# Optimization experiments

Measured on AMD Instinct MI355X. Metric: run time of the kernel, lower is better.

Reference implementation:

```python
import jax, jax.numpy as jnp
import numpy as np

GAMMA = 2.0

def setup_inputs() -> dict:
    key = jax.random.key(0)
    k1, k2, k3, k4 = jax.random.split(key, 4)
    B, N, D, C = 4, 512, 128, 10
    x = jax.random.normal(k1, (B, N, D), dtype=jnp.float32)
    span = jax.random.randint(k2, (B, N, N), 0, C, dtype=jnp.int32)
    seqlen = jax.random.randint(k3, (B,), 1, N + 1, dtype=jnp.int32)
    W = jax.random.truncated_normal(k4, -2.0, 2.0, (D, C), dtype=jnp.float32) * 0.02
    b = jnp.zeros((C,), dtype=jnp.float32)
    return {"x": x, "span": span, "seqlen": seqlen, "W": W, "b": b}

def reference(x, span, seqlen, W, b):
    B, N, D = x.shape
    # pairwise tile-multiply: xx[b,i,j,d] = x[b,i,d] * x[b,j,d]
    xx = x[:, :, None, :] * x[:, None, :, :]            # [B,N,N,D]
    logits = jnp.einsum('bijd,dc->bijc', xx, W) + b     # [B,N,N,C]
    sm = jax.nn.softmax(logits, axis=-1)
    # focal loss: gather prob of true class
    prob = jnp.take_along_axis(sm, span[..., None].astype(jnp.int32), axis=-1)[..., 0]
    loss_map = -jnp.power(1.0 - prob, GAMMA) * jnp.log(prob)  # [B,N,N]
    predict = jnp.argmax(sm, axis=-1).astype(jnp.int32)
    # sequence mask [B,N] -> pairwise [B,N,N]
    row = jnp.arange(N)[None, :] < seqlen[:, None]       # [B,N] bool
    val = row[:, None, :] & row[:, :, None]              # [B,N,N]
    valf = val.astype(jnp.float32)
    seqlen2sum = jnp.sum(jnp.square(seqlen.astype(jnp.float32)))
    loss = jnp.sum(loss_map * valf) / seqlen2sum
    predict = predict * val.astype(jnp.int32)
    accuracy = jnp.sum((predict == span).astype(jnp.float32) * valf) / seqlen2sum
    tp = jnp.sum(((predict == span) & (span > 0)).astype(jnp.float32))
    tn = jnp.sum(((predict != span) & (span > 0)).astype(jnp.float32))
    fp = jnp.sum(((predict > 0) & (span <= 0) & val).astype(jnp.float32))
    return (predict, tp, tn, fp, loss, accuracy)
```

## Files before the change

### kernel.cpp

```cpp
#include <hip/hip_runtime.h>
#include <math.h>

#define NB 4
#define NN 512
#define ND 128
#define NC 10
#define NT 32
#define MREP 2
#define NBLK_M (NB*NT*4)

typedef short    bf16x8 __attribute__((ext_vector_type(8)));
typedef unsigned u32x4  __attribute__((ext_vector_type(4)));
typedef float    f32x4  __attribute__((ext_vector_type(4)));

static __device__ __forceinline__ unsigned pack_trunc(float a, float b) {
    unsigned ua = __builtin_bit_cast(unsigned, a);
    unsigned ub = __builtin_bit_cast(unsigned, b);
    return (ua >> 16) | (ub & 0xFFFF0000u);
}

__global__ __launch_bounds__(256) void w2ner_fused(
    const float* __restrict__ x, const int* __restrict__ span,
    const int* __restrict__ seqlen, const float* __restrict__ Wm,
    const float* __restrict__ bias, float* __restrict__ out,
    float* __restrict__ accum)
{
    __shared__ u32x4 sB[40 * 64];
    __shared__ float sRed[4 * 5];

    const int tid = threadIdx.x;
    const int blk = blockIdx.x;
    const int q  = blk & 3;
    const int Tj = (blk >> 2) & 31;
    const int b  = blk >> 7;
    const int wv = tid >> 6, l = tid & 63;
    const int jl = l & 15, kg = l >> 4;
    const int Ti0 = q * 8 + wv * MREP;
    const int j  = Tj * 16 + jl;
    const int sl = seqlen[b];
    const float* xb = x + (size_t)b * NN * ND;

    int sp[MREP][4];
    #pragma unroll
    for (int m = 0; m < MREP; ++m) {
        const int ib = (Ti0 + m) * 16 + kg * 4;
        #pragma unroll
        for (int r = 0; r < 4; ++r)
            sp[m][r] = span[(size_t)b * NN * NN + (size_t)(ib + r) * NN + j];
    }

    {
        const int d0w = 32 * wv + 8 * kg;
        float xjv[8];
        *(float4*)&xjv[0] = *(const float4*)(xb + (size_t)j * ND + d0w);
        *(float4*)&xjv[4] = *(const float4*)(xb + (size_t)j * ND + d0w + 4);
        u32x4 yw[NC];
        #pragma unroll
        for (int e2 = 0; e2 < 4; ++e2) {
            float wb[20];
            const float4* wp = (const float4*)(Wm + (size_t)(d0w + 2 * e2) * NC);
            #pragma unroll
            for (int t5 = 0; t5 < 5; ++t5) *(float4*)&wb[4 * t5] = wp[t5];
            const float x0 = xjv[2 * e2], x1 = xjv[2 * e2 + 1];
            #pragma unroll
            for (int c = 0; c < NC; ++c)
                yw[c][e2] = pack_trunc(x0 * wb[c], x1 * wb[10 + c]);
        }
        #pragma unroll
        for (int c = 0; c < NC; ++c)
            sB[(wv * NC + c) * 64 + l] = yw[c];
    }
    __syncthreads();

    f32x4 acc[MREP][NC];
    #pragma unroll
    for (int m = 0; m < MREP; ++m)
        #pragma unroll
        for (int c = 0; c < NC; ++c) acc[m][c] = (f32x4){0.f, 0.f, 0.f, 0.f};

    #pragma unroll
    for (int g = 0; g < 4; ++g) {
        const int d0 = 32 * g + 8 * kg;
        bf16x8 ah[MREP], al[MREP];
        #pragma unroll
        for (int m = 0; m < MREP; ++m) {
            const int irow = (Ti0 + m) * 16 + jl;
            float xiv[8];
            *(float4*)&xiv[0] = *(const float4*)(xb + (size_t)irow * ND + d0);
            *(float4*)&xiv[4] = *(const float4*)(xb + (size_t)irow * ND + d0 + 4);
            u32x4 ahw, alw;
            #pragma unroll
            for (int e2 = 0; e2 < 4; ++e2) {
                const float a0 = xiv[2 * e2], a1 = xiv[2 * e2 + 1];
                const unsigned u0 = __builtin_bit_cast(unsigned, a0) & 0xFFFF0000u;
                const unsigned u1 = __builtin_bit_cast(unsigned, a1) & 0xFFFF0000u;
                const float h0 = __builtin_bit_cast(float, u0);
                const float h1 = __builtin_bit_cast(float, u1);
                ahw[e2] = (u0 >> 16) | u1;
                alw[e2] = pack_trunc(a0 - h0, a1 - h1);
            }
            ah[m] = __builtin_bit_cast(bf16x8, ahw);
            al[m] = __builtin_bit_cast(bf16x8, alw);
        }
        #pragma unroll
        for (int c = 0; c < NC; ++c) {
            const bf16x8 bh = __builtin_bit_cast(bf16x8, sB[(g * NC + c) * 64 + l]);
            #pragma unroll
            for (int m = 0; m < MREP; ++m) {
                acc[m][c] = __builtin_amdgcn_mfma_f32_16x16x32_bf16(ah[m], bh, acc[m][c], 0, 0, 0);
                acc[m][c] = __builtin_amdgcn_mfma_f32_16x16x32_bf16(al[m], bh, acc[m][c], 0, 0, 0);
            }
        }
    }

    float lsum = 0.f, accn = 0.f, tpn = 0.f, tnn = 0.f, fpn = 0.f;
    #pragma unroll
    for (int m = 0; m < MREP; ++m) {
        const int ib = (Ti0 + m) * 16 + kg * 4;
        #pragma unroll
        for (int r = 0; r < 4; ++r) {
            const int i = ib + r;
            float L[NC];
            #pragma unroll
            for (int c = 0; c < NC; ++c) L[c] = acc[m][c][r] + bias[c];
            int am = 0; float mx = L[0];
            #pragma unroll
            for (int c = 1; c < NC; ++c) { if (L[c] > mx) { mx = L[c]; am = c; } }
            float e[NC]; float s = 0.f;
            #pragma unroll
            for (int c = 0; c < NC; ++c) { e[c] = __expf(L[c] - mx); s += e[c]; }
            const int spv = sp[m][r];
            float lsp = L[0], esp = e[0];
            #pragma unroll
            for (int c = 1; c < NC; ++c) {
                lsp = (spv == c) ? L[c] : lsp;
                esp = (spv == c) ? e[c] : esp;
            }
            const float inv  = __builtin_amdgcn_rcpf(s);
            const float lp   = (lsp - mx) - __logf(s);
            const float prob = esp * inv;
            const float om   = 1.f - prob;
            const float lm   = -(om * om) * lp;
            const bool v = (i < sl) && (j < sl);
            const int pred = v ? am : 0;
            out[(size_t)b * NN * NN + (size_t)i * NN + j] = (float)pred;
            if (v) { lsum += lm; if (pred == spv) accn += 1.f; }
            if (spv > 0) { if (pred == spv) tpn += 1.f; else tnn += 1.f; }
            else if (pred > 0 && v) fpn += 1.f;
        }
    }

    float vals[5] = { lsum, accn, tpn, tnn, fpn };
    #pragma unroll
    for (int k = 0; k < 5; ++k) {
        float vv = vals[k];
        for (int o = 32; o > 0; o >>= 1) vv += __shfl_down(vv, o);
        vals[k] = vv;
    }
    if (l == 0) {
        #pragma unroll
        for (int k = 0; k < 5; ++k) sRed[wv * 5 + k] = vals[k];
    }
    __syncthreads();
    if (tid < 5) {
        float t = sRed[tid] + sRed[5 + tid] + sRed[10 + tid] + sRed[15 + tid];
        accum[(size_t)blk * 5 + tid] = t;
    }
}

__global__ __launch_bounds__(256) void w2ner_final(
    const int* __restrict__ seqlen, const float* __restrict__ accum,
    float* __restrict__ out)
{
    __shared__ float sP[4][5];
    const int tid = threadIdx.x;
    float part[5] = {0.f, 0.f, 0.f, 0.f, 0.f};
    for (int r = tid; r < NBLK_M; r += 256) {
        #pragma unroll
        for (int k = 0; k < 5; ++k) part[k] += accum[(size_t)r * 5 + k];
    }
    #pragma unroll
    for (int k = 0; k < 5; ++k) {
        float v = part[k];
        for (int o = 32; o > 0; o >>= 1) v += __shfl_down(v, o);
        part[k] = v;
    }
    const int wave = tid >> 6;
    const int lane = tid & 63;
    if (lane == 0) {
        #pragma unroll
        for (int k = 0; k < 5; ++k) sP[wave][k] = part[k];
    }
    __syncthreads();
    if (tid == 0) {
        float t[5];
        #pragma unroll
        for (int k = 0; k < 5; ++k) t[k] = sP[0][k] + sP[1][k] + sP[2][k] + sP[3][k];
        float s2 = 0.f;
        for (int k = 0; k < NB; ++k) { float s = (float)seqlen[k]; s2 += s * s; }
        const size_t base = (size_t)NB * NN * NN;
        out[base + 0] = t[2];
        out[base + 1] = t[3];
        out[base + 2] = t[4];
        out[base + 3] = t[0] / s2;
        out[base + 4] = t[1] / s2;
    }
}

extern "C" void kernel_launch(void* const* d_in, const int* in_sizes, int n_in,
                              void* d_out, int out_size, void* d_ws, size_t ws_size,
                              hipStream_t stream) {
    const float* x      = (const float*)d_in[0];
    const int*   span   = (const int*)d_in[1];
    const int*   seqlen = (const int*)d_in[2];
    const float* Wm     = (const float*)d_in[3];
    const float* bias   = (const float*)d_in[4];
    float* out   = (float*)d_out;
    float* accum = (float*)d_ws;

    w2ner_fused<<<dim3(NBLK_M), 256, 0, stream>>>(x, span, seqlen, Wm, bias, out, accum);
    w2ner_final<<<1, 256, 0, stream>>>(seqlen, accum, out);
}
```

Baseline: 23.90 us.

## Fuse final reduction via last-block counter and compute B operand in registers

```diff
diff --git a/kernel.cpp b/kernel.cpp
--- a/kernel.cpp
+++ b/kernel.cpp
@@ -23,11 +23,10 @@
     const float* __restrict__ x, const int* __restrict__ span,
     const int* __restrict__ seqlen, const float* __restrict__ Wm,
     const float* __restrict__ bias, float* __restrict__ out,
-    float* __restrict__ accum)
+    float* __restrict__ accum, unsigned* __restrict__ counter)
 {
-    __shared__ u32x4 sB[40 * 64];
     __shared__ float sRed[4 * 5];
-
+    __shared__ unsigned sLast;
     const int tid = threadIdx.x;
     const int blk = blockIdx.x;
     const int q  = blk & 3;
@@ -39,6 +38,7 @@
     const int j  = Tj * 16 + jl;
     const int sl = seqlen[b];
     const float* xb = x + (size_t)b * NN * ND;
+    const size_t sb = (size_t)b * NN * NN;
 
     int sp[MREP][4];
     #pragma unroll
@@ -46,41 +46,21 @@
         const int ib = (Ti0 + m) * 16 + kg * 4;
         #pragma unroll
         for (int r = 0; r < 4; ++r)
-            sp[m][r] = span[(size_t)b * NN * NN + (size_t)(ib + r) * NN + j];
-    }
-
-    {
-        const int d0w = 32 * wv + 8 * kg;
-        float xjv[8];
-        *(float4*)&xjv[0] = *(const float4*)(xb + (size_t)j * ND + d0w);
-        *(float4*)&xjv[4] = *(const float4*)(xb + (size_t)j * ND + d0w + 4);
-        u32x4 yw[NC];
-        #pragma unroll
-        for (int e2 = 0; e2 < 4; ++e2) {
-            float wb[20];
-            const float4* wp = (const float4*)(Wm + (size_t)(d0w + 2 * e2) * NC);
-            #pragma unroll
-            for (int t5 = 0; t5 < 5; ++t5) *(float4*)&wb[4 * t5] = wp[t5];
-            const float x0 = xjv[2 * e2], x1 = xjv[2 * e2 + 1];
-            #pragma unroll
-            for (int c = 0; c < NC; ++c)
-                yw[c][e2] = pack_trunc(x0 * wb[c], x1 * wb[10 + c]);
-        }
-        #pragma unroll
-        for (int c = 0; c < NC; ++c)
-            sB[(wv * NC + c) * 64 + l] = yw[c];
-    }
-    __syncthreads();
+            sp[m][r] = span[sb + (size_t)(ib + r) * NN + j];
+    }
 
     f32x4 acc[MREP][NC];
     #pragma unroll
-    for (int m = 0; m < MREP; ++m)
-        #pragma unroll
-        for (int c = 0; c < NC; ++c) acc[m][c] = (f32x4){0.f, 0.f, 0.f, 0.f};
+    for (int c = 0; c < NC; ++c) {
+        const float bc = bias[c];
+        #pragma unroll
+        for (int m = 0; m < MREP; ++m) acc[m][c] = (f32x4){bc, bc, bc, bc};
+    }
 
     #pragma unroll
     for (int g = 0; g < 4; ++g) {
         const int d0 = 32 * g + 8 * kg;
+
         bf16x8 ah[MREP], al[MREP];
         #pragma unroll
         for (int m = 0; m < MREP; ++m) {
@@ -94,17 +74,33 @@
                 const float a0 = xiv[2 * e2], a1 = xiv[2 * e2 + 1];
                 const unsigned u0 = __builtin_bit_cast(unsigned, a0) & 0xFFFF0000u;
                 const unsigned u1 = __builtin_bit_cast(unsigned, a1) & 0xFFFF0000u;
-                const float h0 = __builtin_bit_cast(float, u0);
-                const float h1 = __builtin_bit_cast(float, u1);
                 ahw[e2] = (u0 >> 16) | u1;
-                alw[e2] = pack_trunc(a0 - h0, a1 - h1);
+                alw[e2] = pack_trunc(a0 - __builtin_bit_cast(float, u0),
+                                     a1 - __builtin_bit_cast(float, u1));
             }
             ah[m] = __builtin_bit_cast(bf16x8, ahw);
             al[m] = __builtin_bit_cast(bf16x8, alw);
         }
+
+        float xjv[8];
+        *(float4*)&xjv[0] = *(const float4*)(xb + (size_t)j * ND + d0);
+        *(float4*)&xjv[4] = *(const float4*)(xb + (size_t)j * ND + d0 + 4);
+        u32x4 yw[NC];
+        #pragma unroll
+        for (int e2 = 0; e2 < 4; ++e2) {
+            float wb[20];
+            const float4* wp = (const float4*)(Wm + (size_t)(d0 + 2 * e2) * NC);
+            #pragma unroll
+            for (int t5 = 0; t5 < 5; ++t5) *(float4*)&wb[4 * t5] = wp[t5];
+            const float x0 = xjv[2 * e2], x1 = xjv[2 * e2 + 1];
+            #pragma unroll
+            for (int c = 0; c < NC; ++c)
+                yw[c][e2] = pack_trunc(x0 * wb[c], x1 * wb[10 + c]);
+        }
+
         #pragma unroll
         for (int c = 0; c < NC; ++c) {
-            const bf16x8 bh = __builtin_bit_cast(bf16x8, sB[(g * NC + c) * 64 + l]);
+            const bf16x8 bh = __builtin_bit_cast(bf16x8, yw[c]);
             #pragma unroll
             for (int m = 0; m < MREP; ++m) {
                 acc[m][c] = __builtin_amdgcn_mfma_f32_16x16x32_bf16(ah[m], bh, acc[m][c], 0, 0, 0);
@@ -122,7 +118,7 @@
             const int i = ib + r;
             float L[NC];
             #pragma unroll
-            for (int c = 0; c < NC; ++c) L[c] = acc[m][c][r] + bias[c];
+            for (int c = 0; c < NC; ++c) L[c] = acc[m][c][r];
             int am = 0; float mx = L[0];
             #pragma unroll
             for (int c = 1; c < NC; ++c) { if (L[c] > mx) { mx = L[c]; am = c; } }
@@ -143,7 +139,7 @@
             const float lm   = -(om * om) * lp;
             const bool v = (i < sl) && (j < sl);
             const int pred = v ? am : 0;
-            out[(size_t)b * NN * NN + (size_t)i * NN + j] = (float)pred;
+            out[sb + (size_t)i * NN + j] = (float)pred;
             if (v) { lsum += lm; if (pred == spv) accn += 1.f; }
             if (spv > 0) { if (pred == spv) tpn += 1.f; else tnn += 1.f; }
             else if (pred > 0 && v) fpn += 1.f;
@@ -163,47 +159,46 @@
     }
     __syncthreads();
     if (tid < 5) {
-        float t = sRed[tid] + sRed[5 + tid] + sRed[10 + tid] + sRed[15 + tid];
-        accum[(size_t)blk * 5 + tid] = t;
-    }
-}
-
-__global__ __launch_bounds__(256) void w2ner_final(
-    const int* __restrict__ seqlen, const float* __restrict__ accum,
-    float* __restrict__ out)
-{
-    __shared__ float sP[4][5];
-    const int tid = threadIdx.x;
-    float part[5] = {0.f, 0.f, 0.f, 0.f, 0.f};
-    for (int r = tid; r < NBLK_M; r += 256) {
-        #pragma unroll
-        for (int k = 0; k < 5; ++k) part[k] += accum[(size_t)r * 5 + k];
-    }
-    #pragma unroll
-    for (int k = 0; k < 5; ++k) {
-        float v = part[k];
-        for (int o = 32; o > 0; o >>= 1) v += __shfl_down(v, o);
-        part[k] = v;
-    }
-    const int wave = tid >> 6;
-    const int lane = tid & 63;
-    if (lane == 0) {
-        #pragma unroll
-        for (int k = 0; k < 5; ++k) sP[wave][k] = part[k];
-    }
+        accum[(size_t)blk * 5 + tid] =
+            sRed[tid] + sRed[5 + tid] + sRed[10 + tid] + sRed[15 + tid];
+    }
+
+    __threadfence();
+    if (tid == 0) sLast = (atomicAdd(counter, 1u) == NBLK_M - 1u) ? 1u : 0u;
     __syncthreads();
-    if (tid == 0) {
-        float t[5];
-        #pragma unroll
-        for (int k = 0; k < 5; ++k) t[k] = sP[0][k] + sP[1][k] + sP[2][k] + sP[3][k];
-        float s2 = 0.f;
-        for (int k = 0; k < NB; ++k) { float s = (float)seqlen[k]; s2 += s * s; }
-        const size_t base = (size_t)NB * NN * NN;
-        out[base + 0] = t[2];
-        out[base + 1] = t[3];
-        out[base + 2] = t[4];
-        out[base + 3] = t[0] / s2;
-        out[base + 4] = t[1] / s2;
+    if (sLast) {
+        __threadfence();
+        float part[5] = {0.f, 0.f, 0.f, 0.f, 0.f};
+        for (int r2 = tid; r2 < NBLK_M; r2 += 256) {
+            #pragma unroll
+            for (int k = 0; k < 5; ++k) part[k] += accum[(size_t)r2 * 5 + k];
+        }
+        #pragma unroll
+        for (int k = 0; k < 5; ++k) {
+            float vv = part[k];
+            for (int o = 32; o > 0; o >>= 1) vv += __shfl_down(vv, o);
+            part[k] = vv;
+        }
+        __syncthreads();
+        if (l == 0) {
+            #pragma unroll
+            for (int k = 0; k < 5; ++k) sRed[wv * 5 + k] = part[k];
+        }
+        __syncthreads();
+        if (tid == 0) {
+            float t[5];
+            #pragma unroll
+            for (int k = 0; k < 5; ++k)
+                t[k] = sRed[k] + sRed[5 + k] + sRed[10 + k] + sRed[15 + k];
+            float s2 = 0.f;
+            for (int k = 0; k < NB; ++k) { float s = (float)seqlen[k]; s2 += s * s; }
+            const size_t base = (size_t)NB * NN * NN;
+            out[base + 0] = t[2];
+            out[base + 1] = t[3];
+            out[base + 2] = t[4];
+            out[base + 3] = t[0] / s2;
+            out[base + 4] = t[1] / s2;
+        }
     }
 }
 
@@ -216,8 +211,12 @@
     const float* Wm     = (const float*)d_in[3];
     const float* bias   = (const float*)d_in[4];
     float* out   = (float*)d_out;
-    float* accum = (float*)d_ws;
-
-    w2ner_fused<<<dim3(NBLK_M), 256, 0, stream>>>(x, span, seqlen, Wm, bias, out, accum);
-    w2ner_final<<<1, 256, 0, stream>>>(seqlen, accum, out);
+
+    char* ws = (char*)d_ws;
+    float*    accum   = (float*)ws;
+    unsigned* counter = (unsigned*)(ws + NBLK_M * 5 * sizeof(float));
+
+    hipMemsetAsync(counter, 0, sizeof(unsigned), stream);
+    w2ner_fused<<<dim3(NBLK_M), 256, 0, stream>>>(x, span, seqlen, Wm, bias,
+                                                  out, accum, counter);
 }
```

Result: slower. 66.60 us (+178.7%).

## Split D-reduction across wave pairs and double block count

Applied to the files above, without the earlier changes.

```diff
diff --git a/kernel.cpp b/kernel.cpp
--- a/kernel.cpp
+++ b/kernel.cpp
@@ -6,8 +6,7 @@
 #define ND 128
 #define NC 10
 #define NT 32
-#define MREP 2
-#define NBLK_M (NB*NT*4)
+#define NBLK_M (NB*NT*8)
 
 typedef short    bf16x8 __attribute__((ext_vector_type(8)));
 typedef unsigned u32x4  __attribute__((ext_vector_type(4)));
@@ -25,65 +24,47 @@
     const float* __restrict__ bias, float* __restrict__ out,
     float* __restrict__ accum)
 {
-    __shared__ u32x4 sB[40 * 64];
+    __shared__ f32x4 sEx[NC][2][64];
     __shared__ float sRed[4 * 5];
 
     const int tid = threadIdx.x;
     const int blk = blockIdx.x;
-    const int q  = blk & 3;
-    const int Tj = (blk >> 2) & 31;
-    const int b  = blk >> 7;
+    const int b   = blk >> 8;
+    const int rem = blk & 255;
+    const int Tj  = rem >> 3;
+    const int ig  = rem & 7;
     const int wv = tid >> 6, l = tid & 63;
+    const int pair = wv >> 1, h = wv & 1;
     const int jl = l & 15, kg = l >> 4;
-    const int Ti0 = q * 8 + wv * MREP;
+    const int Ti0 = ig * 4 + pair * 2;
+    const int Tf  = Ti0 + h;
     const int j  = Tj * 16 + jl;
     const int sl = seqlen[b];
     const float* xb = x + (size_t)b * NN * ND;
-
-    int sp[MREP][4];
-    #pragma unroll
-    for (int m = 0; m < MREP; ++m) {
-        const int ib = (Ti0 + m) * 16 + kg * 4;
-        #pragma unroll
-        for (int r = 0; r < 4; ++r)
-            sp[m][r] = span[(size_t)b * NN * NN + (size_t)(ib + r) * NN + j];
-    }
-
-    {
-        const int d0w = 32 * wv + 8 * kg;
-        float xjv[8];
-        *(float4*)&xjv[0] = *(const float4*)(xb + (size_t)j * ND + d0w);
-        *(float4*)&xjv[4] = *(const float4*)(xb + (size_t)j * ND + d0w + 4);
-        u32x4 yw[NC];
-        #pragma unroll
-        for (int e2 = 0; e2 < 4; ++e2) {
-            float wb[20];
-            const float4* wp = (const float4*)(Wm + (size_t)(d0w + 2 * e2) * NC);
-            #pragma unroll
-            for (int t5 = 0; t5 < 5; ++t5) *(float4*)&wb[4 * t5] = wp[t5];
-            const float x0 = xjv[2 * e2], x1 = xjv[2 * e2 + 1];
-            #pragma unroll
-            for (int c = 0; c < NC; ++c)
-                yw[c][e2] = pack_trunc(x0 * wb[c], x1 * wb[10 + c]);
-        }
-        #pragma unroll
-        for (int c = 0; c < NC; ++c)
-            sB[(wv * NC + c) * 64 + l] = yw[c];
-    }
-    __syncthreads();
-
-    f32x4 acc[MREP][NC];
-    #pragma unroll
-    for (int m = 0; m < MREP; ++m)
-        #pragma unroll
-        for (int c = 0; c < NC; ++c) acc[m][c] = (f32x4){0.f, 0.f, 0.f, 0.f};
-
-    #pragma unroll
-    for (int g = 0; g < 4; ++g) {
+    const size_t sb = (size_t)b * NN * NN;
+
+    const int ibf = Tf * 16 + kg * 4;
+    int sp[4];
+    #pragma unroll
+    for (int r = 0; r < 4; ++r)
+        sp[r] = span[sb + (size_t)(ibf + r) * NN + j];
+
+    f32x4 acc[2][NC];
+    #pragma unroll
+    for (int c = 0; c < NC; ++c) {
+        const float bc = (h == 0) ? bias[c] : 0.f;
+        acc[0][c] = (f32x4){bc, bc, bc, bc};
+        acc[1][c] = (f32x4){bc, bc, bc, bc};
+    }
+
+    #pragma unroll
+    for (int gi = 0; gi < 2; ++gi) {
+        const int g  = 2 * h + gi;
         const int d0 = 32 * g + 8 * kg;
-        bf16x8 ah[MREP], al[MREP];
-        #pragma unroll
-        for (int m = 0; m < MREP; ++m) {
+
+        bf16x8 ah[2], al[2];
+        #pragma unroll
+        for (int m = 0; m < 2; ++m) {
             const int irow = (Ti0 + m) * 16 + jl;
             float xiv[8];
             *(float4*)&xiv[0] = *(const float4*)(xb + (size_t)irow * ND + d0);
@@ -94,60 +75,94 @@
                 const float a0 = xiv[2 * e2], a1 = xiv[2 * e2 + 1];
                 const unsigned u0 = __builtin_bit_cast(unsigned, a0) & 0xFFFF0000u;
                 const unsigned u1 = __builtin_bit_cast(unsigned, a1) & 0xFFFF0000u;
-                const float h0 = __builtin_bit_cast(float, u0);
-                const float h1 = __builtin_bit_cast(float, u1);
                 ahw[e2] = (u0 >> 16) | u1;
-                alw[e2] = pack_trunc(a0 - h0, a1 - h1);
+                alw[e2] = pack_trunc(a0 - __builtin_bit_cast(float, u0),
+                                     a1 - __builtin_bit_cast(float, u1));
             }
             ah[m] = __builtin_bit_cast(bf16x8, ahw);
             al[m] = __builtin_bit_cast(bf16x8, alw);
         }
+
+        float xjv[8];
+        *(float4*)&xjv[0] = *(const float4*)(xb + (size_t)j * ND + d0);
+        *(float4*)&xjv[4] = *(const float4*)(xb + (size_t)j * ND + d0 + 4);
+        u32x4 yw[NC];
+        #pragma unroll
+        for (int e2 = 0; e2 < 4; ++e2) {
+            float wb[20];
+            const float4* wp = (const float4*)(Wm + (size_t)(d0 + 2 * e2) * NC);
+            #pragma unroll
+            for (int t5 = 0; t5 < 5; ++t5) *(float4*)&wb[4 * t5] = wp[t5];
+            const float x0 = xjv[2 * e2], x1 = xjv[2 * e2 + 1];
+            #pragma unroll
+            for (int c = 0; c < NC; ++c)
+                yw[c][e2] = pack_trunc(x0 * wb[c], x1 * wb[10 + c]);
+        }
+
         #pragma unroll
         for (int c = 0; c < NC; ++c) {
-            const bf16x8 bh = __builtin_bit_cast(bf16x8, sB[(g * NC + c) * 64 + l]);
-            #pragma unroll
-            for (int m = 0; m < MREP; ++m) {
+            const bf16x8 bh = __builtin_bit_cast(bf16x8, yw[c]);
+            #pragma unroll
+            for (int m = 0; m < 2; ++m) {
                 acc[m][c] = __builtin_amdgcn_mfma_f32_16x16x32_bf16(ah[m], bh, acc[m][c], 0, 0, 0);
                 acc[m][c] = __builtin_amdgcn_mfma_f32_16x16x32_bf16(al[m], bh, acc[m][c], 0, 0, 0);
             }
         }
     }
 
+    if (h == 0) {
+        #pragma unroll
+        for (int c = 0; c < NC; ++c) sEx[c][pair][l] = acc[1][c];
+    }
+    __syncthreads();
+    if (h == 1) {
+        #pragma unroll
+        for (int c = 0; c < NC; ++c) {
+            const f32x4 t = sEx[c][pair][l];
+            acc[1][c] += t;
+            sEx[c][pair][l] = acc[0][c];
+        }
+    }
+    __syncthreads();
+    if (h == 0) {
+        #pragma unroll
+        for (int c = 0; c < NC; ++c) acc[0][c] += sEx[c][pair][l];
+    } else {
+        #pragma unroll
+        for (int c = 0; c < NC; ++c) acc[0][c] = acc[1][c];
+    }
+
     float lsum = 0.f, accn = 0.f, tpn = 0.f, tnn = 0.f, fpn = 0.f;
     #pragma unroll
-    for (int m = 0; m < MREP; ++m) {
-        const int ib = (Ti0 + m) * 16 + kg * 4;
-        #pragma unroll
-        for (int r = 0; r < 4; ++r) {
-            const int i = ib + r;
-            float L[NC];
-            #pragma unroll
-            for (int c = 0; c < NC; ++c) L[c] = acc[m][c][r] + bias[c];
-            int am = 0; float mx = L[0];
-            #pragma unroll
-            for (int c = 1; c < NC; ++c) { if (L[c] > mx) { mx = L[c]; am = c; } }
-            float e[NC]; float s = 0.f;
-            #pragma unroll
-            for (int c = 0; c < NC; ++c) { e[c] = __expf(L[c] - mx); s += e[c]; }
-            const int spv = sp[m][r];
-            float lsp = L[0], esp = e[0];
-            #pragma unroll
-            for (int c = 1; c < NC; ++c) {
-                lsp = (spv == c) ? L[c] : lsp;
-                esp = (spv == c) ? e[c] : esp;
-            }
-            const float inv  = __builtin_amdgcn_rcpf(s);
-            const float lp   = (lsp - mx) - __logf(s);
-            const float prob = esp * inv;
-            const float om   = 1.f - prob;
-            const float lm   = -(om * om) * lp;
-            const bool v = (i < sl) && (j < sl);
-            const int pred = v ? am : 0;
-            out[(size_t)b * NN * NN + (size_t)i * NN + j] = (float)pred;
-            if (v) { lsum += lm; if (pred == spv) accn += 1.f; }
-            if (spv > 0) { if (pred == spv) tpn += 1.f; else tnn += 1.f; }
-            else if (pred > 0 && v) fpn += 1.f;
-        }
+    for (int r = 0; r < 4; ++r) {
+        const int i = ibf + r;
+        float L[NC];
+        #pragma unroll
+        for (int c = 0; c < NC; ++c) L[c] = acc[0][c][r];
+        int am = 0; float mx = L[0];
+        #pragma unroll
+        for (int c = 1; c < NC; ++c) { if (L[c] > mx) { mx = L[c]; am = c; } }
+        float e[NC]; float s = 0.f;
+        #pragma unroll
+        for (int c = 0; c < NC; ++c) { e[c] = __expf(L[c] - mx); s += e[c]; }
+        const int spv = sp[r];
+        float lsp = L[0], esp = e[0];
+        #pragma unroll
+        for (int c = 1; c < NC; ++c) {
+            lsp = (spv == c) ? L[c] : lsp;
+            esp = (spv == c) ? e[c] : esp;
+        }
+        const float inv  = __builtin_amdgcn_rcpf(s);
+        const float lp   = (lsp - mx) - __logf(s);
+        const float prob = esp * inv;
+        const float om   = 1.f - prob;
+        const float lm   = -(om * om) * lp;
+        const bool v = (i < sl) && (j < sl);
+        const int pred = v ? am : 0;
+        out[sb + (size_t)i * NN + j] = (float)pred;
+        if (v) { lsum += lm; if (pred == spv) accn += 1.f; }
+        if (spv > 0) { if (pred == spv) tpn += 1.f; else tnn += 1.f; }
+        else if (pred > 0 && v) fpn += 1.f;
     }
 
     float vals[5] = { lsum, accn, tpn, tnn, fpn };
@@ -163,8 +178,8 @@
     }
     __syncthreads();
     if (tid < 5) {
-        float t = sRed[tid] + sRed[5 + tid] + sRed[10 + tid] + sRed[15 + tid];
-        accum[(size_t)blk * 5 + tid] = t;
+        accum[(size_t)blk * 5 + tid] =
+            sRed[tid] + sRed[5 + tid] + sRed[10 + tid] + sRed[15 + tid];
     }
 }
 
```

Result: slower. 27.83 us (+16.5%).

## Drop split-bf16 low term, compute B operand in registers, transpose partials

Applied to the files above, without the earlier changes.

```diff
diff --git a/kernel.cpp b/kernel.cpp
--- a/kernel.cpp
+++ b/kernel.cpp
@@ -13,10 +13,10 @@
 typedef unsigned u32x4  __attribute__((ext_vector_type(4)));
 typedef float    f32x4  __attribute__((ext_vector_type(4)));
 
-static __device__ __forceinline__ unsigned pack_trunc(float a, float b) {
-    unsigned ua = __builtin_bit_cast(unsigned, a);
-    unsigned ub = __builtin_bit_cast(unsigned, b);
-    return (ua >> 16) | (ub & 0xFFFF0000u);
+static __device__ __forceinline__ unsigned pack_bf2(float a, float b) {
+    unsigned short la = __builtin_bit_cast(unsigned short, (__bf16)a);
+    unsigned short hb = __builtin_bit_cast(unsigned short, (__bf16)b);
+    return (unsigned)la | ((unsigned)hb << 16);
 }
 
 __global__ __launch_bounds__(256) void w2ner_fused(
@@ -25,9 +25,7 @@
     const float* __restrict__ bias, float* __restrict__ out,
     float* __restrict__ accum)
 {
-    __shared__ u32x4 sB[40 * 64];
     __shared__ float sRed[4 * 5];
-
     const int tid = threadIdx.x;
     const int blk = blockIdx.x;
     const int q  = blk & 3;
@@ -39,6 +37,7 @@
     const int j  = Tj * 16 + jl;
     const int sl = seqlen[b];
     const float* xb = x + (size_t)b * NN * ND;
+    const size_t sb = (size_t)b * NN * NN;
 
     int sp[MREP][4];
     #pragma unroll
@@ -46,70 +45,57 @@
         const int ib = (Ti0 + m) * 16 + kg * 4;
         #pragma unroll
         for (int r = 0; r < 4; ++r)
-            sp[m][r] = span[(size_t)b * NN * NN + (size_t)(ib + r) * NN + j];
-    }
-
-    {
-        const int d0w = 32 * wv + 8 * kg;
-        float xjv[8];
-        *(float4*)&xjv[0] = *(const float4*)(xb + (size_t)j * ND + d0w);
-        *(float4*)&xjv[4] = *(const float4*)(xb + (size_t)j * ND + d0w + 4);
-        u32x4 yw[NC];
-        #pragma unroll
-        for (int e2 = 0; e2 < 4; ++e2) {
-            float wb[20];
-            const float4* wp = (const float4*)(Wm + (size_t)(d0w + 2 * e2) * NC);
-            #pragma unroll
-            for (int t5 = 0; t5 < 5; ++t5) *(float4*)&wb[4 * t5] = wp[t5];
-            const float x0 = xjv[2 * e2], x1 = xjv[2 * e2 + 1];
-            #pragma unroll
-            for (int c = 0; c < NC; ++c)
-                yw[c][e2] = pack_trunc(x0 * wb[c], x1 * wb[10 + c]);
-        }
-        #pragma unroll
-        for (int c = 0; c < NC; ++c)
-            sB[(wv * NC + c) * 64 + l] = yw[c];
-    }
-    __syncthreads();
+            sp[m][r] = span[sb + (size_t)(ib + r) * NN + j];
+    }
 
     f32x4 acc[MREP][NC];
     #pragma unroll
-    for (int m = 0; m < MREP; ++m)
-        #pragma unroll
-        for (int c = 0; c < NC; ++c) acc[m][c] = (f32x4){0.f, 0.f, 0.f, 0.f};
+    for (int c = 0; c < NC; ++c) {
+        const float bc = bias[c];
+        #pragma unroll
+        for (int m = 0; m < MREP; ++m) acc[m][c] = (f32x4){bc, bc, bc, bc};
+    }
 
     #pragma unroll
     for (int g = 0; g < 4; ++g) {
         const int d0 = 32 * g + 8 * kg;
-        bf16x8 ah[MREP], al[MREP];
+
+        bf16x8 ah[MREP];
         #pragma unroll
         for (int m = 0; m < MREP; ++m) {
             const int irow = (Ti0 + m) * 16 + jl;
             float xiv[8];
             *(float4*)&xiv[0] = *(const float4*)(xb + (size_t)irow * ND + d0);
             *(float4*)&xiv[4] = *(const float4*)(xb + (size_t)irow * ND + d0 + 4);
-            u32x4 ahw, alw;
-            #pragma unroll
-            for (int e2 = 0; e2 < 4; ++e2) {
-                const float a0 = xiv[2 * e2], a1 = xiv[2 * e2 + 1];
-                const unsigned u0 = __builtin_bit_cast(unsigned, a0) & 0xFFFF0000u;
-                const unsigned u1 = __builtin_bit_cast(unsigned, a1) & 0xFFFF0000u;
-                const float h0 = __builtin_bit_cast(float, u0);
-                const float h1 = __builtin_bit_cast(float, u1);
-                ahw[e2] = (u0 >> 16) | u1;
-                alw[e2] = pack_trunc(a0 - h0, a1 - h1);
-            }
+            u32x4 ahw;
+            #pragma unroll
+            for (int e2 = 0; e2 < 4; ++e2)
+                ahw[e2] = pack_bf2(xiv[2 * e2], xiv[2 * e2 + 1]);
             ah[m] = __builtin_bit_cast(bf16x8, ahw);
-            al[m] = __builtin_bit_cast(bf16x8, alw);
-        }
+        }
+
+        float xjv[8];
+        *(float4*)&xjv[0] = *(const float4*)(xb + (size_t)j * ND + d0);
+        *(float4*)&xjv[4] = *(const float4*)(xb + (size_t)j * ND + d0 + 4);
+        u32x4 yw[NC];
+        #pragma unroll
+        for (int e2 = 0; e2 < 4; ++e2) {
+            float wb[20];
+            const float4* wp = (const float4*)(Wm + (size_t)(d0 + 2 * e2) * NC);
+            #pragma unroll
+            for (int t5 = 0; t5 < 5; ++t5) *(float4*)&wb[4 * t5] = wp[t5];
+            const float x0 = xjv[2 * e2], x1 = xjv[2 * e2 + 1];
+            #pragma unroll
+            for (int c = 0; c < NC; ++c)
+                yw[c][e2] = pack_bf2(x0 * wb[c], x1 * wb[10 + c]);
+        }
+
         #pragma unroll
         for (int c = 0; c < NC; ++c) {
-            const bf16x8 bh = __builtin_bit_cast(bf16x8, sB[(g * NC + c) * 64 + l]);
-            #pragma unroll
-            for (int m = 0; m < MREP; ++m) {
+            const bf16x8 bh = __builtin_bit_cast(bf16x8, yw[c]);
+            #pragma unroll
+            for (int m = 0; m < MREP; ++m)
                 acc[m][c] = __builtin_amdgcn_mfma_f32_16x16x32_bf16(ah[m], bh, acc[m][c], 0, 0, 0);
-                acc[m][c] = __builtin_amdgcn_mfma_f32_16x16x32_bf16(al[m], bh, acc[m][c], 0, 0, 0);
-            }
         }
     }
 
@@ -122,7 +108,7 @@
             const int i = ib + r;
             float L[NC];
             #pragma unroll
-            for (int c = 0; c < NC; ++c) L[c] = acc[m][c][r] + bias[c];
+            for (int c = 0; c < NC; ++c) L[c] = acc[m][c][r];
             int am = 0; float mx = L[0];
             #pragma unroll
             for (int c = 1; c < NC; ++c) { if (L[c] > mx) { mx = L[c]; am = c; } }
@@ -143,7 +129,7 @@
             const float lm   = -(om * om) * lp;
             const bool v = (i < sl) && (j < sl);
             const int pred = v ? am : 0;
-            out[(size_t)b * NN * NN + (size_t)i * NN + j] = (float)pred;
+            out[sb + (size_t)i * NN + j] = (float)pred;
             if (v) { lsum += lm; if (pred == spv) accn += 1.f; }
             if (spv > 0) { if (pred == spv) tpn += 1.f; else tnn += 1.f; }
             else if (pred > 0 && v) fpn += 1.f;
@@ -163,22 +149,20 @@
     }
     __syncthreads();
     if (tid < 5) {
-        float t = sRed[tid] + sRed[5 + tid] + sRed[10 + tid] + sRed[15 + tid];
-        accum[(size_t)blk * 5 + tid] = t;
-    }
-}
-
-__global__ __launch_bounds__(256) void w2ner_final(
+        accum[(size_t)tid * NBLK_M + blk] =
+            sRed[tid] + sRed[5 + tid] + sRed[10 + tid] + sRed[15 + tid];
+    }
+}
+
+__global__ __launch_bounds__(512) void w2ner_final(
     const int* __restrict__ seqlen, const float* __restrict__ accum,
     float* __restrict__ out)
 {
-    __shared__ float sP[4][5];
+    __shared__ float sP[8][5];
     const int tid = threadIdx.x;
-    float part[5] = {0.f, 0.f, 0.f, 0.f, 0.f};
-    for (int r = tid; r < NBLK_M; r += 256) {
-        #pragma unroll
-        for (int k = 0; k < 5; ++k) part[k] += accum[(size_t)r * 5 + k];
-    }
+    float part[5];
+    #pragma unroll
+    for (int k = 0; k < 5; ++k) part[k] = accum[(size_t)k * NBLK_M + tid];
     #pragma unroll
     for (int k = 0; k < 5; ++k) {
         float v = part[k];
@@ -195,7 +179,12 @@
     if (tid == 0) {
         float t[5];
         #pragma unroll
-        for (int k = 0; k < 5; ++k) t[k] = sP[0][k] + sP[1][k] + sP[2][k] + sP[3][k];
+        for (int k = 0; k < 5; ++k) {
+            float s = 0.f;
+            #pragma unroll
+            for (int w = 0; w < 8; ++w) s += sP[w][k];
+            t[k] = s;
+        }
         float s2 = 0.f;
         for (int k = 0; k < NB; ++k) { float s = (float)seqlen[k]; s2 += s * s; }
         const size_t base = (size_t)NB * NN * NN;
@@ -219,5 +208,5 @@
     float* accum = (float*)d_ws;
 
     w2ner_fused<<<dim3(NBLK_M), 256, 0, stream>>>(x, span, seqlen, Wm, bias, out, accum);
-    w2ner_final<<<1, 256, 0, stream>>>(seqlen, accum, out);
-}
+    w2ner_final<<<1, 512, 0, stream>>>(seqlen, accum, out);
+}
```

Measured after the change: 24.18 us. About the same (+1.2%).
